# Optimization experiments

Hardware: AMD Instinct MI355X
Metric: run time of the kernel (lower is better)

The kernel has to match this reference:

```python
import jax, jax.numpy as jnp
import numpy as np

B, T, D = 4, 8192, 768
H = 12
HD = D // H
DFF = 4 * D
EPS_ATT = 1e-6
EPS_LN = 1e-5


def _layernorm(x, g, b):
    mu = jnp.mean(x, axis=-1, keepdims=True)
    var = jnp.mean(jnp.square(x - mu), axis=-1, keepdims=True)
    return (x - mu) * jax.lax.rsqrt(var + EPS_LN) * g + b


def setup_inputs() -> dict:
    key = jax.random.key(0)
    ks = jax.random.split(key, 12)
    s = 1.0 / np.sqrt(D)
    sf = 1.0 / np.sqrt(DFF)
    return {
        "x": jax.random.normal(ks[0], (B, T, D), jnp.float32),
        "Wq": jax.random.uniform(ks[1], (D, D), jnp.float32, -s, s),
        "Wk": jax.random.uniform(ks[2], (D, D), jnp.float32, -s, s),
        "Wv": jax.random.uniform(ks[3], (D, D), jnp.float32, -s, s),
        "Wo": jax.random.uniform(ks[4], (D, D), jnp.float32, -s, s),
        "bo": jax.random.uniform(ks[5], (D,), jnp.float32, -s, s),
        "ln1_g": jnp.ones((D,), jnp.float32),
        "ln1_b": jnp.zeros((D,), jnp.float32),
        "ln2_g": jnp.ones((D,), jnp.float32),
        "ln2_b": jnp.zeros((D,), jnp.float32),
        "W1": jax.random.uniform(ks[6], (D, DFF), jnp.float32, -s, s),
        "b1": jax.random.uniform(ks[7], (DFF,), jnp.float32, -s, s),
        "W2": jax.random.uniform(ks[8], (DFF, D), jnp.float32, -sf, sf),
        "b2": jax.random.uniform(ks[9], (D,), jnp.float32, -sf, sf),
    }


def reference(x, Wq, Wk, Wv, Wo, bo, ln1_g, ln1_b, ln2_g, ln2_b, W1, b1, W2, b2):
    h = x
    xn = _layernorm(x, ln1_g, ln1_b)
    # QKV projections -> [B, H, T, HD]
    def heads(w):
        return (xn @ w).reshape(B, T, H, HD).transpose(0, 2, 1, 3)
    Q = jax.nn.elu(heads(Wq)) + 1.0
    K = jax.nn.elu(heads(Wk)) + 1.0
    V = heads(Wv)
    # linear attention: KV outer-product sum and K_sum normalization
    KV = jnp.einsum('bhtd,bhte->bhde', K, V)      # [B,H,HD,HD]
    K_sum = K.sum(axis=2)                          # [B,H,HD]
    Z = jnp.einsum('bhtd,bhd->bht', Q, K_sum) + EPS_ATT
    ctx = jnp.einsum('bhtd,bhde->bhte', Q, KV) / Z[..., None]
    att = ctx.transpose(0, 2, 1, 3).reshape(B, T, D) @ Wo + bo
    x = att + h  # dropout is identity in eval
    h = x
    xn = _layernorm(x, ln2_g, ln2_b)
    ff = jax.nn.gelu(xn @ W1 + b1, approximate=False) @ W2 + b2
    return ff + h
```

## Files before the change

kernel.cpp:

```cpp
#include <hip/hip_runtime.h>
#include <math.h>


#define DEV __device__ __forceinline__

typedef __attribute__((ext_vector_type(8))) short s16x8;
typedef __attribute__((ext_vector_type(4))) float f32x4;

static constexpr int    Bb   = 4;
static constexpr int    Tt   = 8192;
static constexpr int    Dd   = 768;
static constexpr int    Hh   = 12;
static constexpr size_t Mrows = (size_t)Bb * Tt;

DEV float bf2f(unsigned short u) {
    union { unsigned int i; float f; } c; c.i = ((unsigned int)u) << 16; return c.f;
}
DEV unsigned short f2bf(float f) {
    union { float f; unsigned int i; } c; c.f = f;
    unsigned int r = c.i + 0x7fffu + ((c.i >> 16) & 1u);
    return (unsigned short)(r >> 16);
}

DEV void gload16(const unsigned short* g, void* l) {
    __builtin_amdgcn_global_load_lds(
        (const __attribute__((address_space(1))) void*)g,
        (__attribute__((address_space(3))) void*)l, 16, 0, 0);
}

__global__ __launch_bounds__(256)
void transpose_f2b(const float* __restrict__ in, unsigned short* __restrict__ out,
                   int R, int C) {
    __shared__ float tile[32][33];
    const int c0 = blockIdx.x * 32, r0 = blockIdx.y * 32;
    const int tx = threadIdx.x, ty = threadIdx.y;
    #pragma unroll
    for (int i = 0; i < 32; i += 8)
        tile[ty + i][tx] = in[(size_t)(r0 + ty + i) * C + c0 + tx];
    __syncthreads();
    #pragma unroll
    for (int i = 0; i < 32; i += 8)
        out[(size_t)(c0 + ty + i) * R + r0 + tx] = f2bf(tile[tx][ty + i]);
}

template <int BF16IN>
__global__ __launch_bounds__(256)
void ln_kernel(const void* __restrict__ xin, const float* __restrict__ g,
               const float* __restrict__ bvec, unsigned short* __restrict__ out) {
    __shared__ float red[4];
    const int tid = threadIdx.x;
    const size_t base = (size_t)blockIdx.x * Dd;
    float v[3];
    #pragma unroll
    for (int i = 0; i < 3; ++i) {
        const size_t idx = base + tid + i * 256;
        if (BF16IN) v[i] = bf2f(((const unsigned short*)xin)[idx]);
        else        v[i] = ((const float*)xin)[idx];
    }
    float s = v[0] + v[1] + v[2];
    #pragma unroll
    for (int o = 32; o >= 1; o >>= 1) s += __shfl_xor(s, o);
    if ((tid & 63) == 0) red[tid >> 6] = s;
    __syncthreads();
    s = red[0] + red[1] + red[2] + red[3];
    const float mu = s * (1.0f / Dd);
    __syncthreads();
    float q = 0.f;
    #pragma unroll
    for (int i = 0; i < 3; ++i) { const float d = v[i] - mu; q += d * d; }
    #pragma unroll
    for (int o = 32; o >= 1; o >>= 1) q += __shfl_xor(q, o);
    if ((tid & 63) == 0) red[tid >> 6] = q;
    __syncthreads();
    q = red[0] + red[1] + red[2] + red[3];
    const float rstd = rsqrtf(q * (1.0f / Dd) + 1e-5f);
    #pragma unroll
    for (int i = 0; i < 3; ++i) {
        const int c = tid + i * 256;
        out[base + c] = f2bf((v[i] - mu) * rstd * g[c] + bvec[c]);
    }
}

#define EPI_QKV  0
#define EPI_X2   1
#define EPI_GELU 2
#define EPI_OUT1 3
#define EPI_OUT2 4

template <int EPI, int K, int PB>
__global__ __launch_bounds__(256, 4)
void gemm97(const unsigned short* __restrict__ A,
            const unsigned short* __restrict__ BT,
            const float* __restrict__ bias,
            const void* __restrict__ res,
            void* __restrict__ out, int N) {
    const int NTile = N >> 7;
    const int nwg = gridDim.x;
    int wg = blockIdx.x;
    wg = (wg & 7) * (nwg >> 3) + (wg >> 3);
    const int nt = wg % NTile, mt = wg / NTile;
    const int m0 = mt * 128, n0 = nt * 128;
    const int tid = threadIdx.x;
    const int lane = tid & 63, w = tid >> 6;
    const int wm = w >> 1, wn = w & 1;
    const int l15 = lane & 15, lk = lane >> 4;

    __shared__ __align__(16) char lds[16384];

    const unsigned short* BTb = PB ? (BT + (size_t)(m0 >> 13) * 768 * 768) : BT;

    const int srow = lane >> 2;
    const int gsrc = (lane & 3) ^ ((lane >> 3) & 3);
    const int swb  = ((l15 >> 1) & 3) << 4;

    f32x4 acc[4][4] = {};

    for (int kt = 0; kt < K; kt += 32) {
        #pragma unroll
        for (int j = 0; j < 4; ++j) {
            const int grp = w * 4 + j;
            const unsigned short* src = (grp < 8)
                ? A   + (size_t)(m0 + grp * 16 + srow) * K + kt + gsrc * 8
                : BTb + (size_t)(n0 + (grp - 8) * 16 + srow) * K + kt + gsrc * 8;
            gload16(src, lds + grp * 1024);
        }
        __syncthreads();

        const char* bA = lds + (wm * 64) * 64;
        const char* bB = lds + 8192 + (wn * 64) * 64;
        s16x8 af[4], bf[4];
        #pragma unroll
        for (int i = 0; i < 4; ++i) {
            af[i] = *(const s16x8*)(bA + (i * 16 + l15) * 64 + ((lk << 4) ^ swb));
            bf[i] = *(const s16x8*)(bB + (i * 16 + l15) * 64 + ((lk << 4) ^ swb));
        }
        #pragma unroll
        for (int i = 0; i < 4; ++i)
            #pragma unroll
            for (int j = 0; j < 4; ++j)
                acc[i][j] = __builtin_amdgcn_mfma_f32_16x16x32_bf16(af[i], bf[j], acc[i][j], 0, 0, 0);
        __syncthreads();
    }

    #pragma unroll
    for (int mi = 0; mi < 4; ++mi) {
        #pragma unroll
        for (int nj = 0; nj < 4; ++nj) {
            const int col = n0 + wn * 64 + nj * 16 + l15;
            #pragma unroll
            for (int r = 0; r < 4; ++r) {
                const int row = m0 + wm * 64 + mi * 16 + lk * 4 + r;
                float v = acc[mi][nj][r];
                if (EPI == EPI_QKV) {
                    const int which = col / 768;
                    const int cc = col - which * 768;
                    if (which < 2) v = (v > 0.f) ? (v + 1.f) : __expf(v);
                    ((unsigned short*)out)[(size_t)which * (Mrows * Dd) + (size_t)row * Dd + cc] = f2bf(v);
                } else if (EPI == EPI_X2) {
                    v += bias[col] + ((const float*)res)[(size_t)row * N + col];
                    ((unsigned short*)out)[(size_t)row * N + col] = f2bf(v);
                } else if (EPI == EPI_GELU) {
                    v += bias[col];
                    v = 0.5f * v * (1.0f + erff(v * 0.70710678118654752f));
                    ((unsigned short*)out)[(size_t)row * N + col] = f2bf(v);
                } else if (EPI == EPI_OUT1) {
                    v += bias[col] + bf2f(((const unsigned short*)res)[(size_t)row * N + col]);
                    ((float*)out)[(size_t)row * N + col] = v;
                } else {
                    ((float*)out)[(size_t)row * N + col] += v;
                }
            }
        }
    }
}

__global__ __launch_bounds__(256)
void kv_partial(const unsigned short* __restrict__ Km, const unsigned short* __restrict__ Vm,
                float* __restrict__ part, float* __restrict__ pksum) {
    const int ck = blockIdx.x, bh = blockIdx.y;
    const int b = bh / Hh, h = bh - b * Hh;
    const int tid = threadIdx.x;
    const int e = tid & 63, dg = tid >> 6;
    __shared__ float sK[32][64], sV[32][64];
    float acc[16] = {};
    float ksacc = 0.f;
    const size_t rowbase = ((size_t)b * Tt + (size_t)ck * 1024) * Dd + h * 64;
    const int rw = tid >> 3, cv = (tid & 7) * 8;
    for (int ts = 0; ts < 1024; ts += 32) {
        const s16x8 k8 = *(const s16x8*)(Km + rowbase + (size_t)(ts + rw) * Dd + cv);
        const s16x8 v8 = *(const s16x8*)(Vm + rowbase + (size_t)(ts + rw) * Dd + cv);
        float kf[8], vf[8];
        #pragma unroll
        for (int j = 0; j < 8; ++j) {
            kf[j] = bf2f((unsigned short)k8[j]);
            vf[j] = bf2f((unsigned short)v8[j]);
        }
        __syncthreads();
        *(float4*)(&sK[rw][cv])     = *(const float4*)&kf[0];
        *(float4*)(&sK[rw][cv + 4]) = *(const float4*)&kf[4];
        *(float4*)(&sV[rw][cv])     = *(const float4*)&vf[0];
        *(float4*)(&sV[rw][cv + 4]) = *(const float4*)&vf[4];
        __syncthreads();
        #pragma unroll 4
        for (int tt = 0; tt < 32; ++tt) {
            const float vv = sV[tt][e];
            const float4* kp = (const float4*)(&sK[tt][dg * 16]);
            const float4 k0 = kp[0], k1 = kp[1], k2 = kp[2], k3 = kp[3];
            acc[0]  += k0.x * vv; acc[1]  += k0.y * vv; acc[2]  += k0.z * vv; acc[3]  += k0.w * vv;
            acc[4]  += k1.x * vv; acc[5]  += k1.y * vv; acc[6]  += k1.z * vv; acc[7]  += k1.w * vv;
            acc[8]  += k2.x * vv; acc[9]  += k2.y * vv; acc[10] += k2.z * vv; acc[11] += k2.w * vv;
            acc[12] += k3.x * vv; acc[13] += k3.y * vv; acc[14] += k3.z * vv; acc[15] += k3.w * vv;
        }
        if (dg == 0) {
            #pragma unroll 4
            for (int tt = 0; tt < 32; ++tt) ksacc += sK[tt][e];
        }
    }
    float* op = part + ((size_t)bh * 8 + ck) * 4096 + (size_t)dg * 16 * 64 + e;
    #pragma unroll
    for (int i = 0; i < 16; ++i) op[(size_t)i * 64] = acc[i];
    if (dg == 0) pksum[((size_t)bh * 8 + ck) * 64 + e] = ksacc;
}

__global__ __launch_bounds__(256)
void kv_reduce(const float* __restrict__ part, const float* __restrict__ pksum,
               float* __restrict__ kv, float* __restrict__ ksum) {
    const int bh = blockIdx.x;
    const int tid = threadIdx.x;
    #pragma unroll
    for (int j = 0; j < 16; ++j) {
        const int i = j * 256 + tid;
        float s = 0.f;
        #pragma unroll
        for (int c = 0; c < 8; ++c) s += part[((size_t)bh * 8 + c) * 4096 + i];
        kv[(size_t)bh * 4096 + i] = s;
    }
    if (tid < 64) {
        float s = 0.f;
        #pragma unroll
        for (int c = 0; c < 8; ++c) s += pksum[((size_t)bh * 8 + c) * 64 + tid];
        ksum[(size_t)bh * 64 + tid] = s;
    }
}

__global__ __launch_bounds__(256)
void qscale_kernel(unsigned short* __restrict__ Q, const float* __restrict__ ksum) {
    const int row = blockIdx.x;
    const int b = row >> 13;
    const int tid = threadIdx.x, lane = tid & 63;
    const size_t base = (size_t)row * Dd;
    #pragma unroll
    for (int i = 0; i < 3; ++i) {
        const int c = i * 256 + tid;
        const int h = c >> 6;
        const float q = bf2f(Q[base + c]);
        float zp = q * ksum[((size_t)b * Hh + h) * 64 + lane];
        #pragma unroll
        for (int o = 32; o >= 1; o >>= 1) zp += __shfl_xor(zp, o);
        const float zi = 1.0f / (zp + 1e-6f);
        Q[base + c] = f2bf(q * zi);
    }
}

__global__ __launch_bounds__(256)
void w2_build(const float* __restrict__ kvf, const unsigned short* __restrict__ woT,
              unsigned short* __restrict__ W2T) {
    const int bh = blockIdx.x, ny = blockIdx.y;
    const int b = bh / Hh, h = bh - b * Hh;
    __shared__ float sKV[64][65];
    const int tid = threadIdx.x;
    for (int i = tid; i < 4096; i += 256) sKV[i >> 6][i & 63] = kvf[(size_t)bh * 4096 + i];
    __syncthreads();
    const int d = tid & 63, ng = tid >> 6;
    #pragma unroll 4
    for (int i = 0; i < 48; ++i) {
        const int n = ny * 192 + i * 4 + ng;
        const unsigned short* wr = woT + (size_t)n * Dd + h * 64;
        float a = 0.f;
        #pragma unroll
        for (int e = 0; e < 64; ++e) a += bf2f(wr[e]) * sKV[d][e];
        W2T[((size_t)b * Dd + n) * Dd + h * 64 + d] = f2bf(a);
    }
}

extern "C" void kernel_launch(void* const* d_in, const int* in_sizes, int n_in,
                              void* d_out, int out_size, void* d_ws, size_t ws_size,
                              hipStream_t stream) {
    (void)in_sizes; (void)n_in; (void)out_size; (void)ws_size;
    const float* x    = (const float*)d_in[0];
    const float* Wq   = (const float*)d_in[1];
    const float* Wk   = (const float*)d_in[2];
    const float* Wv   = (const float*)d_in[3];
    const float* Wo   = (const float*)d_in[4];
    const float* bo   = (const float*)d_in[5];
    const float* ln1g = (const float*)d_in[6];
    const float* ln1b = (const float*)d_in[7];
    const float* ln2g = (const float*)d_in[8];
    const float* ln2b = (const float*)d_in[9];
    const float* W1   = (const float*)d_in[10];
    const float* b1   = (const float*)d_in[11];
    const float* W2   = (const float*)d_in[12];
    const float* b2   = (const float*)d_in[13];
    float* outp = (float*)d_out;

    char* ws = (char*)d_ws;
    const size_t SZ = Mrows * Dd * 2;
    unsigned short* xn = (unsigned short*)(ws + 0);
    unsigned short* Qb = (unsigned short*)(ws + SZ);
    unsigned short* Kb = (unsigned short*)(ws + 2 * SZ);
    unsigned short* Vb = (unsigned short*)(ws + 3 * SZ);
    char* p = ws + 4 * SZ;
    float* part  = (float*)p;  p += (size_t)48 * 8 * 4096 * 4;
    float* kvf   = (float*)p;  p += (size_t)48 * 4096 * 4;
    float* ksumf = (float*)p;  p += (size_t)48 * 64 * 4;
    unsigned short* wqkvT = (unsigned short*)p; p += (size_t)2304 * 768 * 2;
    unsigned short* woT   = (unsigned short*)p; p += (size_t)768 * 768 * 2;
    unsigned short* w1T   = (unsigned short*)p; p += (size_t)3072 * 768 * 2;
    unsigned short* w2aT  = (unsigned short*)p; p += (size_t)768 * 1536 * 2;
    unsigned short* w2bT  = (unsigned short*)p; p += (size_t)768 * 1536 * 2;
    float* pksum = (float*)p;  p += (size_t)48 * 8 * 64 * 4;
    unsigned short* W2T = (unsigned short*)part;
    unsigned short* ff1 = Qb;
    unsigned short* x2b = Vb;

    const dim3 blk(256);
    const dim3 tb(32, 8);

    transpose_f2b<<<dim3(24, 24), tb, 0, stream>>>(Wq, wqkvT, 768, 768);
    transpose_f2b<<<dim3(24, 24), tb, 0, stream>>>(Wk, wqkvT + 589824, 768, 768);
    transpose_f2b<<<dim3(24, 24), tb, 0, stream>>>(Wv, wqkvT + 2 * 589824, 768, 768);
    transpose_f2b<<<dim3(24, 24), tb, 0, stream>>>(Wo, woT, 768, 768);
    transpose_f2b<<<dim3(96, 24), tb, 0, stream>>>(W1, w1T, 768, 3072);
    transpose_f2b<<<dim3(24, 48), tb, 0, stream>>>(W2, w2aT, 1536, 768);
    transpose_f2b<<<dim3(24, 48), tb, 0, stream>>>(W2 + (size_t)1536 * 768, w2bT, 1536, 768);

    ln_kernel<0><<<32768, blk, 0, stream>>>(x, ln1g, ln1b, xn);

    gemm97<EPI_QKV, 768, 0><<<4608, blk, 0, stream>>>(xn, wqkvT, nullptr, nullptr, Qb, 2304);

    kv_partial<<<dim3(8, 48), blk, 0, stream>>>(Kb, Vb, part, pksum);
    kv_reduce<<<48, blk, 0, stream>>>(part, pksum, kvf, ksumf);

    qscale_kernel<<<32768, blk, 0, stream>>>(Qb, ksumf);
    w2_build<<<dim3(48, 4), blk, 0, stream>>>(kvf, woT, W2T);

    gemm97<EPI_X2, 768, 1><<<1536, blk, 0, stream>>>(Qb, W2T, bo, x, x2b, 768);

    ln_kernel<1><<<32768, blk, 0, stream>>>(x2b, ln2g, ln2b, xn);

    gemm97<EPI_GELU, 768, 0><<<3072, blk, 0, stream>>>(xn, w1T, b1, nullptr, ff1, 1536);
    gemm97<EPI_OUT1, 1536, 0><<<1536, blk, 0, stream>>>(ff1, w2aT, b2, x2b, outp, 768);
    gemm97<EPI_GELU, 768, 0><<<3072, blk, 0, stream>>>(xn, w1T + (size_t)1536 * 768,
                                                       b1 + 1536, nullptr, ff1, 1536);
    gemm97<EPI_OUT2, 1536, 0><<<1536, blk, 0, stream>>>(ff1, w2bT, nullptr, nullptr, outp, 768);
}
```

Measured before the change: 996.7 us.

## Double-buffer GEMM LDS tiles and merge weight transposes into one launch

The GEMM now uses two LDS buffers, issuing the next K-tile's global-to-LDS loads before computing on the current tile, with one barrier per iteration. This aims to overlap memory latency with MFMA work, at the cost of doubled LDS per block. The seven weight-transpose launches are fused into a single kernel that dispatches on block index, to cut launch overhead.

New measurement: 1.213 ms. 1.22x slower.

```diff
diff --git a/kernel.cpp b/kernel.cpp
--- a/kernel.cpp
+++ b/kernel.cpp
@@ -29,10 +29,23 @@
 }
 
 __global__ __launch_bounds__(256)
-void transpose_f2b(const float* __restrict__ in, unsigned short* __restrict__ out,
-                   int R, int C) {
+void transpose_all(const float* __restrict__ Wq, const float* __restrict__ Wk,
+                   const float* __restrict__ Wv, const float* __restrict__ Wo,
+                   const float* __restrict__ W1, const float* __restrict__ W2,
+                   unsigned short* __restrict__ wqkvT, unsigned short* __restrict__ woT,
+                   unsigned short* __restrict__ w1T, unsigned short* __restrict__ w2aT,
+                   unsigned short* __restrict__ w2bT) {
     __shared__ float tile[32][33];
-    const int c0 = blockIdx.x * 32, r0 = blockIdx.y * 32;
+    int bid = blockIdx.x;
+    const float* in; unsigned short* out; int R, C, gx;
+    if (bid < 576)        { in = Wq; out = wqkvT;           R = 768;  C = 768;  gx = 24; }
+    else if (bid < 1152)  { in = Wk; out = wqkvT + 589824;  R = 768;  C = 768;  gx = 24; bid -= 576; }
+    else if (bid < 1728)  { in = Wv; out = wqkvT + 1179648; R = 768;  C = 768;  gx = 24; bid -= 1152; }
+    else if (bid < 2304)  { in = Wo; out = woT;             R = 768;  C = 768;  gx = 24; bid -= 1728; }
+    else if (bid < 4608)  { in = W1; out = w1T;             R = 768;  C = 3072; gx = 96; bid -= 2304; }
+    else if (bid < 5760)  { in = W2; out = w2aT;            R = 1536; C = 768;  gx = 24; bid -= 4608; }
+    else                  { in = W2 + (size_t)1536 * 768; out = w2bT; R = 1536; C = 768; gx = 24; bid -= 5760; }
+    const int c0 = (bid % gx) * 32, r0 = (bid / gx) * 32;
     const int tx = threadIdx.x, ty = threadIdx.y;
     #pragma unroll
     for (int i = 0; i < 32; i += 8)
@@ -89,11 +102,11 @@
 
 template <int EPI, int K, int PB>
 __global__ __launch_bounds__(256, 4)
-void gemm97(const unsigned short* __restrict__ A,
-            const unsigned short* __restrict__ BT,
-            const float* __restrict__ bias,
-            const void* __restrict__ res,
-            void* __restrict__ out, int N) {
+void gemm97d(const unsigned short* __restrict__ A,
+             const unsigned short* __restrict__ BT,
+             const float* __restrict__ bias,
+             const void* __restrict__ res,
+             void* __restrict__ out, int N) {
     const int NTile = N >> 7;
     const int nwg = gridDim.x;
     int wg = blockIdx.x;
@@ -105,7 +118,7 @@
     const int wm = w >> 1, wn = w & 1;
     const int l15 = lane & 15, lk = lane >> 4;
 
-    __shared__ __align__(16) char lds[16384];
+    __shared__ __align__(16) char lds[32768];
 
     const unsigned short* BTb = PB ? (BT + (size_t)(m0 >> 13) * 768 * 768) : BT;
 
@@ -113,21 +126,28 @@
     const int gsrc = (lane & 3) ^ ((lane >> 3) & 3);
     const int swb  = ((l15 >> 1) & 3) << 4;
 
-    f32x4 acc[4][4] = {};
-
-    for (int kt = 0; kt < K; kt += 32) {
+    auto stage = [&](int kt, int d) {
+        char* base = lds + d * 16384;
         #pragma unroll
         for (int j = 0; j < 4; ++j) {
             const int grp = w * 4 + j;
             const unsigned short* src = (grp < 8)
                 ? A   + (size_t)(m0 + grp * 16 + srow) * K + kt + gsrc * 8
                 : BTb + (size_t)(n0 + (grp - 8) * 16 + srow) * K + kt + gsrc * 8;
-            gload16(src, lds + grp * 1024);
-        }
+            gload16(src, base + grp * 1024);
+        }
+    };
+
+    f32x4 acc[4][4] = {};
+
+    stage(0, 0);
+    int d = 0;
+    for (int kt = 0; kt < K; kt += 32, d ^= 1) {
         __syncthreads();
-
-        const char* bA = lds + (wm * 64) * 64;
-        const char* bB = lds + 8192 + (wn * 64) * 64;
+        if (kt + 32 < K) stage(kt + 32, d ^ 1);
+
+        const char* bA = lds + d * 16384 + (wm * 64) * 64;
+        const char* bB = lds + d * 16384 + 8192 + (wn * 64) * 64;
         s16x8 af[4], bf[4];
         #pragma unroll
         for (int i = 0; i < 4; ++i) {
@@ -139,7 +159,6 @@
             #pragma unroll
             for (int j = 0; j < 4; ++j)
                 acc[i][j] = __builtin_amdgcn_mfma_f32_16x16x32_bf16(af[i], bf[j], acc[i][j], 0, 0, 0);
-        __syncthreads();
     }
 
     #pragma unroll
@@ -326,17 +345,12 @@
     const dim3 blk(256);
     const dim3 tb(32, 8);
 
-    transpose_f2b<<<dim3(24, 24), tb, 0, stream>>>(Wq, wqkvT, 768, 768);
-    transpose_f2b<<<dim3(24, 24), tb, 0, stream>>>(Wk, wqkvT + 589824, 768, 768);
-    transpose_f2b<<<dim3(24, 24), tb, 0, stream>>>(Wv, wqkvT + 2 * 589824, 768, 768);
-    transpose_f2b<<<dim3(24, 24), tb, 0, stream>>>(Wo, woT, 768, 768);
-    transpose_f2b<<<dim3(96, 24), tb, 0, stream>>>(W1, w1T, 768, 3072);
-    transpose_f2b<<<dim3(24, 48), tb, 0, stream>>>(W2, w2aT, 1536, 768);
-    transpose_f2b<<<dim3(24, 48), tb, 0, stream>>>(W2 + (size_t)1536 * 768, w2bT, 1536, 768);
+    transpose_all<<<6912, tb, 0, stream>>>(Wq, Wk, Wv, Wo, W1, W2,
+                                           wqkvT, woT, w1T, w2aT, w2bT);
 
     ln_kernel<0><<<32768, blk, 0, stream>>>(x, ln1g, ln1b, xn);
 
-    gemm97<EPI_QKV, 768, 0><<<4608, blk, 0, stream>>>(xn, wqkvT, nullptr, nullptr, Qb, 2304);
+    gemm97d<EPI_QKV, 768, 0><<<4608, blk, 0, stream>>>(xn, wqkvT, nullptr, nullptr, Qb, 2304);
 
     kv_partial<<<dim3(8, 48), blk, 0, stream>>>(Kb, Vb, part, pksum);
     kv_reduce<<<48, blk, 0, stream>>>(part, pksum, kvf, ksumf);
@@ -344,13 +358,13 @@
     qscale_kernel<<<32768, blk, 0, stream>>>(Qb, ksumf);
     w2_build<<<dim3(48, 4), blk, 0, stream>>>(kvf, woT, W2T);
 
-    gemm97<EPI_X2, 768, 1><<<1536, blk, 0, stream>>>(Qb, W2T, bo, x, x2b, 768);
+    gemm97d<EPI_X2, 768, 1><<<1536, blk, 0, stream>>>(Qb, W2T, bo, x, x2b, 768);
 
     ln_kernel<1><<<32768, blk, 0, stream>>>(x2b, ln2g, ln2b, xn);
 
-    gemm97<EPI_GELU, 768, 0><<<3072, blk, 0, stream>>>(xn, w1T, b1, nullptr, ff1, 1536);
-    gemm97<EPI_OUT1, 1536, 0><<<1536, blk, 0, stream>>>(ff1, w2aT, b2, x2b, outp, 768);
-    gemm97<EPI_GELU, 768, 0><<<3072, blk, 0, stream>>>(xn, w1T + (size_t)1536 * 768,
-                                                       b1 + 1536, nullptr, ff1, 1536);
-    gemm97<EPI_OUT2, 1536, 0><<<1536, blk, 0, stream>>>(ff1, w2bT, nullptr, nullptr, outp, 768);
-}
+    gemm97d<EPI_GELU, 768, 0><<<3072, blk, 0, stream>>>(xn, w1T, b1, nullptr, ff1, 1536);
+    gemm97d<EPI_OUT1, 1536, 0><<<1536, blk, 0, stream>>>(ff1, w2aT, b2, x2b, outp, 768);
+    gemm97d<EPI_GELU, 768, 0><<<3072, blk, 0, stream>>>(xn, w1T + (size_t)1536 * 768,
+                                                        b1 + 1536, nullptr, ff1, 1536);
+    gemm97d<EPI_OUT2, 1536, 0><<<1536, blk, 0, stream>>>(ff1, w2bT, nullptr, nullptr, outp, 768);
+}
```
